# Kernel optimization log

Measured on AMD Instinct MI355X. Metric: run time of the kernel, lower is better.

Reference implementation:

```python
import jax, jax.numpy as jnp
import numpy as np

N = 20000      # nodes
E = 320000     # edges
B = 128        # graphs in batch
DIN = 64       # in_channels == out_channels (residual)
DEDGE = 64     # edge_attr_dim
DINS = 64      # ins_dim
H = 2          # heads
C = 64         # out_channels per head
L = 2          # num_ins (conv layers)
SLOPE = 0.2    # leaky relu negative slope
EPS = 1e-5     # batchnorm eps


def setup_inputs() -> dict:
    key = jax.random.key(0)
    ks = jax.random.split(key, 12)
    s = 0.05  # small glorot-ish init scale
    return {
        "x": jax.random.normal(ks[0], (N, DIN), jnp.float32),
        "edge_index": jax.random.randint(ks[1], (2, E), 0, N),
        "edge_attr": jax.random.normal(ks[2], (E, DEDGE), jnp.float32),
        "instr_vectors": jax.random.normal(ks[3], (L, B, DINS), jnp.float32),
        "batch": jnp.sort(jax.random.randint(ks[4], (N,), 0, B)),
        "W_l": jax.random.normal(ks[5], (L, DIN + DINS, H * C), jnp.float32) * s,
        "W_e": jax.random.normal(ks[6], (L, DEDGE + DINS, H * C), jnp.float32) * s,
        "att_l": jax.random.normal(ks[7], (L, H, C), jnp.float32) * s,
        "att_r": jax.random.normal(ks[8], (L, H, C), jnp.float32) * s,
        "att_e": jax.random.normal(ks[9], (L, H, C), jnp.float32) * s,
        "bias": jnp.zeros((L, C), jnp.float32),
        "bn_gamma": jnp.ones((L - 1, C), jnp.float32),
        "bn_beta": jnp.zeros((L - 1, C), jnp.float32),
    }


def reference(x, edge_index, edge_attr, instr_vectors, batch,
              W_l, W_e, att_l, att_r, att_e, bias, bn_gamma, bn_beta):
    src, dst = edge_index[0], edge_index[1]  # j -> i (source_to_target)
    h = x
    for i in range(L):
        ins = instr_vectors[i]                                   # [B, DINS]
        x_cat = jnp.concatenate([h, ins[batch]], axis=-1)        # [N, DIN+DINS]
        e_cat = jnp.concatenate([edge_attr, ins[batch[src]]], axis=-1)  # [E, ...]
        xl = (x_cat @ W_l[i]).reshape(-1, H, C)                  # [N,H,C] (lin_l == lin_r)
        al = (xl * att_l[i]).sum(-1)                             # [N,H]
        ar = (xl * att_r[i]).sum(-1)                             # [N,H]
        eh = (e_cat @ W_e[i]).reshape(-1, H, C)                  # [E,H,C]
        ae = (eh * att_e[i]).sum(-1)                             # [E,H]
        a = al[src] + ar[dst] + ae                               # [E,H]
        a = jnp.where(a > 0, a, SLOPE * a)                       # leaky relu
        # segment softmax over incoming edges of each target node
        m = jax.ops.segment_max(a, dst, num_segments=N)          # [N,H]
        ex = jnp.exp(a - m[dst])
        ssum = jax.ops.segment_sum(ex, dst, num_segments=N)
        alpha = ex / (ssum[dst] + 1e-16)                         # [E,H]
        out = jax.ops.segment_sum(xl[src] * alpha[:, :, None], dst, num_segments=N)
        out = out.mean(axis=1) + bias[i]                         # concat=False -> head mean
        h = out + h                                              # residual
        if i != L - 1:
            mu = h.mean(axis=0)
            var = ((h - mu) ** 2).mean(axis=0)                   # biased var (BN training)
            h = (h - mu) / jnp.sqrt(var + EPS) * bn_gamma[i] + bn_beta[i]
            h = jax.nn.relu(h)
    return h
```

## Files before the change

kernel.cpp:

```cpp
#include <hip/hip_runtime.h>
#include <math.h>

#define NN 20000
#define NE 320000
#define NB 128
#define SLOPE 0.2f
#define BN_EPS 1e-5f
#define NBLK 79

__device__ __forceinline__ unsigned short f2bf(float f) {
    unsigned int u = __float_as_uint(f);
    unsigned int r = (u + 0x7FFFu + ((u >> 16) & 1u)) >> 16;
    return (unsigned short)r;
}
__device__ __forceinline__ float bf2f(unsigned short h) {
    return __uint_as_float(((unsigned int)h) << 16);
}

__global__ __launch_bounds__(256) void k_hist(const int* __restrict__ dst, int* __restrict__ deg) {
    int e = blockIdx.x * 256 + threadIdx.x;
    if (e < NE) atomicAdd(&deg[dst[e]], 1);
}

__global__ __launch_bounds__(256) void k_scanA(const int* __restrict__ deg, int* __restrict__ bsum) {
    __shared__ int wsum[4];
    int t = threadIdx.x;
    int idx = blockIdx.x * 256 + t;
    int v = (idx < NN) ? deg[idx] : 0;
    for (int off = 32; off > 0; off >>= 1) v += __shfl_xor(v, off);
    if ((t & 63) == 0) wsum[t >> 6] = v;
    __syncthreads();
    if (t == 0) bsum[blockIdx.x] = wsum[0] + wsum[1] + wsum[2] + wsum[3];
}

__global__ __launch_bounds__(64) void k_scanB(const int* __restrict__ bsum, int* __restrict__ boff,
                                              int* __restrict__ rowptr) {
    int l = threadIdx.x;
    int v0 = (l < NBLK) ? bsum[l] : 0;
    int v1 = (64 + l < NBLK) ? bsum[64 + l] : 0;
    int o0 = v0, o1 = v1;
    for (int off = 1; off < 64; off <<= 1) { int u = __shfl_up(v0, off); if (l >= off) v0 += u; }
    int tot0 = __shfl(v0, 63);
    for (int off = 1; off < 64; off <<= 1) { int u = __shfl_up(v1, off); if (l >= off) v1 += u; }
    int tot1 = __shfl(v1, 63);
    if (l < NBLK) boff[l] = v0 - o0;
    if (64 + l < NBLK) boff[64 + l] = tot0 + v1 - o1;
    if (l == 0) rowptr[NN] = tot0 + tot1;
}

__global__ __launch_bounds__(256) void k_scanC(const int* __restrict__ deg, const int* __restrict__ boff,
                                               int* __restrict__ rowptr, int* __restrict__ cursor) {
    __shared__ int wsum[4];
    int t = threadIdx.x, lane = t & 63, w = t >> 6;
    int idx = blockIdx.x * 256 + t;
    int v = (idx < NN) ? deg[idx] : 0;
    int incl = v;
    for (int off = 1; off < 64; off <<= 1) { int u = __shfl_up(incl, off); if (lane >= off) incl += u; }
    if (lane == 63) wsum[w] = incl;
    __syncthreads();
    int pre = 0;
    for (int i = 0; i < w; ++i) pre += wsum[i];
    int excl = incl - v + pre + boff[blockIdx.x];
    if (idx < NN) { rowptr[idx] = excl; cursor[idx] = excl; }
}

__global__ __launch_bounds__(256) void k_p1(const float* __restrict__ We, const float* __restrict__ atte,
                                            float* __restrict__ ve01, float* __restrict__ w2e01) {
    int L = blockIdx.x;
    const float* WeL = We + (size_t)L * 128 * 128;
    const float* aeL = atte + L * 128;
    int t = threadIdx.x;
    int h = (t >> 6) & 1;
    int k = t & 63;
    int row = (t < 128) ? k : (64 + k);
    float acc = 0.f;
    for (int c = 0; c < 64; ++c) acc += WeL[row * 128 + h * 64 + c] * aeL[h * 64 + c];
    if (t < 128) ve01[L * 128 + t] = acc;
    else        w2e01[L * 128 + (t - 128)] = acc;
}

__global__ __launch_bounds__(256) void k_p2both(const float* __restrict__ instr, const float* __restrict__ Wl,
                                                const float* __restrict__ w2e01,
                                                float* __restrict__ insl01, float* __restrict__ ce01) {
    int blk = blockIdx.x, t = threadIdx.x;
    if (blk < 128) {
        int L = blk >> 6;
        int idx = (blk & 63) * 256 + t;
        int b = idx >> 7, j = idx & 127;
        const float* ins = instr + (size_t)L * NB * 64;
        const float* WlL = Wl + (size_t)L * 128 * 128;
        float acc = 0.f;
        for (int k = 0; k < 64; ++k) acc += ins[b * 64 + k] * WlL[(64 + k) * 128 + j];
        insl01[(size_t)L * 16384 + idx] = acc;
    } else {
        int L = blk - 128;
        int b = t >> 1, h = t & 1;
        const float* ins = instr + (size_t)L * NB * 64;
        const float* w2 = w2e01 + L * 128 + h * 64;
        float acc = 0.f;
        for (int k = 0; k < 64; ++k) acc += ins[b * 64 + k] * w2[k];
        ce01[L * 256 + b * 2 + h] = acc;
    }
}

__global__ __launch_bounds__(256) void k_sced(const int* __restrict__ src, const int* __restrict__ dst,
                                              const float* __restrict__ eattr, const float* __restrict__ ve01,
                                              int* __restrict__ cursor,
                                              int* __restrict__ csr_s, int* __restrict__ csr_d,
                                              float4* __restrict__ ae4) {
    __shared__ float sv[256];
    int t = threadIdx.x;
    sv[t] = ve01[t];
    __syncthreads();
    int e = blockIdx.x * 256 + t;
    if (e >= NE) return;
    int s = src[e], d = dst[e];
    const float4* row = (const float4*)(eattr + (size_t)e * 64);
    float a00 = 0.f, a01 = 0.f, a10 = 0.f, a11 = 0.f;
#pragma unroll
    for (int q = 0; q < 16; ++q) {
        float4 f = row[q];
        int k = q * 4;
        a00 += f.x * sv[k] + f.y * sv[k + 1] + f.z * sv[k + 2] + f.w * sv[k + 3];
        a01 += f.x * sv[64 + k] + f.y * sv[64 + k + 1] + f.z * sv[64 + k + 2] + f.w * sv[64 + k + 3];
        a10 += f.x * sv[128 + k] + f.y * sv[128 + k + 1] + f.z * sv[128 + k + 2] + f.w * sv[128 + k + 3];
        a11 += f.x * sv[192 + k] + f.y * sv[192 + k + 1] + f.z * sv[192 + k + 2] + f.w * sv[192 + k + 3];
    }
    int pos = atomicAdd(&cursor[d], 1);
    csr_s[pos] = s;
    csr_d[pos] = d;
    ae4[pos] = make_float4(a00, a01, a10, a11);
}

__global__ __launch_bounds__(256) void k_node(const float* __restrict__ hcur, const float* __restrict__ Wl,
                                              const float* __restrict__ insl, const int* __restrict__ batch,
                                              const float* __restrict__ attl, const float* __restrict__ attr_,
                                              const float2* __restrict__ ce2,
                                              const float* __restrict__ scsh, int use_bn,
                                              unsigned short* __restrict__ xlh,
                                              float* __restrict__ alc, float* __restrict__ ar) {
    __shared__ float sh[8 * 64];
    int t = threadIdx.x;
    int row0 = blockIdx.x * 8;
    for (int idx = t; idx < 512; idx += 256) {
        int r = idx >> 6, k = idx & 63;
        int n = row0 + r;
        float hv = (n < NN) ? hcur[n * 64 + k] : 0.f;
        if (use_bn) hv = fmaxf(hv * scsh[k] + scsh[64 + k], 0.f);
        sh[idx] = hv;
    }
    __syncthreads();
    int w = t >> 6, lane = t & 63;
    int h = w & 1;
    int rbase = (w >> 1) * 4;
    int j = h * 64 + lane;
    float attlv = attl[j];
    float attrv = attr_[j];
    float acc0 = 0.f, acc1 = 0.f, acc2 = 0.f, acc3 = 0.f;
    for (int k = 0; k < 64; ++k) {
        float wv = Wl[k * 128 + j];
        acc0 += sh[(rbase + 0) * 64 + k] * wv;
        acc1 += sh[(rbase + 1) * 64 + k] * wv;
        acc2 += sh[(rbase + 2) * 64 + k] * wv;
        acc3 += sh[(rbase + 3) * 64 + k] * wv;
    }
    float accs[4] = {acc0, acc1, acc2, acc3};
    for (int rr = 0; rr < 4; ++rr) {
        int n = row0 + rbase + rr;
        if (n >= NN) break;
        int b = batch[n];
        float v = accs[rr] + insl[b * 128 + j];
        xlh[(size_t)n * 128 + j] = f2bf(v);
        float pl = v * attlv, pr = v * attrv;
        for (int off = 32; off > 0; off >>= 1) {
            pl += __shfl_xor(pl, off);
            pr += __shfl_xor(pr, off);
        }
        if (lane == 0) {
            float2 cb = ce2[b];
            alc[n * 2 + h] = pl + (h ? cb.y : cb.x);
            ar[n * 2 + h] = pr;
        }
    }
}

__global__ __launch_bounds__(256) void k_attnexp(const int* __restrict__ csr_s, const int* __restrict__ csr_d,
                                                 const float4* __restrict__ ae4, int layer,
                                                 const float2* __restrict__ alc2, const float2* __restrict__ ar2,
                                                 int4* __restrict__ rec) {
    int p = blockIdx.x * 256 + threadIdx.x;
    if (p >= NE) return;
    int s = csr_s[p], d = csr_d[p];
    float4 ae = ae4[p];
    float2 a_l = alc2[s];
    float2 a_r = ar2[d];
    float a0 = a_l.x + a_r.x + (layer ? ae.z : ae.x);
    float a1 = a_l.y + a_r.y + (layer ? ae.w : ae.y);
    a0 = (a0 > 0.f) ? a0 : SLOPE * a0;
    a1 = (a1 > 0.f) ? a1 : SLOPE * a1;
    rec[p] = make_int4(s, __float_as_int(__expf(a0)), __float_as_int(__expf(a1)), 0);
}

__global__ __launch_bounds__(256) void k_gather(const int* __restrict__ rowptr, const int4* __restrict__ rec,
                                                const unsigned int* __restrict__ xl32,
                                                const float* __restrict__ bias, const float* __restrict__ hprev,
                                                const float* __restrict__ scsh, int use_bn,
                                                float* __restrict__ hnew) {
    int t = threadIdx.x;
    int w = t >> 6, lane = t & 63;
    int n = blockIdx.x * 4 + w;
    if (n >= NN) return;
    int r0 = rowptr[n], r1 = rowptr[n + 1];
    float acc0 = 0.f, acc1 = 0.f, ss = 0.f;
    const unsigned int* xlp = xl32 + lane;
#pragma unroll 4
    for (int p = r0; p < r1; ++p) {
        int4 r = rec[p];
        float ex = (lane < 32) ? __int_as_float(r.y) : __int_as_float(r.z);
        unsigned int pr = xlp[(size_t)r.x * 64];
        ss += ex;
        acc0 += ex * bf2f((unsigned short)(pr & 0xFFFFu));
        acc1 += ex * bf2f((unsigned short)(pr >> 16));
    }
    float inv = 1.f / (ss + 1e-16f);
    acc0 *= inv; acc1 *= inv;
    float o0 = 0.5f * (acc0 + __shfl_xor(acc0, 32));
    float o1 = 0.5f * (acc1 + __shfl_xor(acc1, 32));
    if (lane < 32) {
        float2 hv = ((const float2*)(hprev + (size_t)n * 64))[lane];
        if (use_bn) {
            float2 sc = ((const float2*)scsh)[lane];
            float2 sf = ((const float2*)(scsh + 64))[lane];
            hv.x = fmaxf(hv.x * sc.x + sf.x, 0.f);
            hv.y = fmaxf(hv.y * sc.y + sf.y, 0.f);
        }
        float2 bv = ((const float2*)bias)[lane];
        float2 o;
        o.x = o0 + bv.x + hv.x;
        o.y = o1 + bv.y + hv.y;
        ((float2*)(hnew + (size_t)n * 64))[lane] = o;
    }
}

__global__ __launch_bounds__(256) void k_bnstat(const float* __restrict__ hbuf,
                                                float* __restrict__ part, float* __restrict__ partsq) {
    __shared__ float sA[256], sB[256];
    int t = threadIdx.x;
    int c = t & 63, r = t >> 6;
    int n0 = blockIdx.x * 80;
    float s = 0.f, s2 = 0.f;
    for (int i = 0; i < 20; ++i) {
        float v = hbuf[(size_t)(n0 + i * 4 + r) * 64 + c];
        s += v; s2 += v * v;
    }
    sA[t] = s; sB[t] = s2;
    __syncthreads();
    if (t < 64) {
        part[blockIdx.x * 64 + t]   = sA[t] + sA[t + 64] + sA[t + 128] + sA[t + 192];
        partsq[blockIdx.x * 64 + t] = sB[t] + sB[t + 64] + sB[t + 128] + sB[t + 192];
    }
}

__global__ __launch_bounds__(256) void k_bnred(const float* __restrict__ part, const float* __restrict__ partsq,
                                               const float* __restrict__ gamma, const float* __restrict__ beta,
                                               float* __restrict__ scsh) {
    __shared__ float sA[256], sB[256];
    int t = threadIdx.x;
    int c = t & 63, q = t >> 6;
    float s = 0.f, s2 = 0.f;
    for (int j = q; j < 250; j += 4) { s += part[j * 64 + c]; s2 += partsq[j * 64 + c]; }
    sA[t] = s; sB[t] = s2;
    __syncthreads();
    if (t < 64) {
        float su = sA[t] + sA[t + 64] + sA[t + 128] + sA[t + 192];
        float sq = sB[t] + sB[t + 64] + sB[t + 128] + sB[t + 192];
        float mu = su * (1.f / NN);
        float var = sq * (1.f / NN) - mu * mu;
        float sc = gamma[t] * rsqrtf(var + BN_EPS);
        scsh[t] = sc;
        scsh[64 + t] = beta[t] - mu * sc;
    }
}

extern "C" void kernel_launch(void* const* d_in, const int* in_sizes, int n_in,
                              void* d_out, int out_size, void* d_ws, size_t ws_size,
                              hipStream_t stream) {
    (void)in_sizes; (void)n_in; (void)out_size; (void)ws_size;
    const float* x     = (const float*)d_in[0];
    const int*   eidx  = (const int*)d_in[1];
    const float* eattr = (const float*)d_in[2];
    const float* instr = (const float*)d_in[3];
    const int*   batch = (const int*)d_in[4];
    const float* W_l   = (const float*)d_in[5];
    const float* W_e   = (const float*)d_in[6];
    const float* att_l = (const float*)d_in[7];
    const float* att_r = (const float*)d_in[8];
    const float* att_e = (const float*)d_in[9];
    const float* bias  = (const float*)d_in[10];
    const float* bn_g  = (const float*)d_in[11];
    const float* bn_b  = (const float*)d_in[12];
    float* out = (float*)d_out;

    const int* src = eidx;
    const int* dst = eidx + NE;

    char* ws = (char*)d_ws;
    float4* ae4     = (float4*)ws;     ws += (size_t)NE * 16;
    int4*   rec     = (int4*)ws;       ws += (size_t)NE * 16;
    unsigned short* xlh = (unsigned short*)ws; ws += (size_t)NN * 128 * 2;
    int*    csr_s   = (int*)ws;        ws += (size_t)NE * 4;
    int*    csr_d   = (int*)ws;        ws += (size_t)NE * 4;
    int*    deg     = (int*)ws;        ws += NN * 4;
    int*    rowptr  = (int*)ws;        ws += (NN + 1) * 4 + 4;
    int*    cursor  = (int*)ws;        ws += NN * 4;
    int*    bsum    = (int*)ws;        ws += 80 * 4;
    int*    boff    = (int*)ws;        ws += 80 * 4;
    float*  alc     = (float*)ws;      ws += NN * 2 * 4;
    float*  ar      = (float*)ws;      ws += NN * 2 * 4;
    float*  insl01  = (float*)ws;      ws += 2 * 128 * 128 * 4;
    float*  ve01    = (float*)ws;      ws += 256 * 4;
    float*  w2e01   = (float*)ws;      ws += 256 * 4;
    float*  ce01    = (float*)ws;      ws += 2 * 256 * 4;
    float*  hbuf    = (float*)ws;      ws += (size_t)NN * 64 * 4;
    float*  part    = (float*)ws;      ws += 250 * 64 * 4;
    float*  partsq  = (float*)ws;      ws += 250 * 64 * 4;
    float*  scsh    = (float*)ws;      ws += 128 * 4;

    hipMemsetAsync(deg, 0, NN * 4, stream);
    k_hist<<<(NE + 255) / 256, 256, 0, stream>>>(dst, deg);
    k_scanA<<<NBLK, 256, 0, stream>>>(deg, bsum);
    k_scanB<<<1, 64, 0, stream>>>(bsum, boff, rowptr);
    k_scanC<<<NBLK, 256, 0, stream>>>(deg, boff, rowptr, cursor);

    k_p1<<<2, 256, 0, stream>>>(W_e, att_e, ve01, w2e01);
    k_sced<<<(NE + 255) / 256, 256, 0, stream>>>(src, dst, eattr, ve01, cursor, csr_s, csr_d, ae4);
    k_p2both<<<130, 256, 0, stream>>>(instr, W_l, w2e01, insl01, ce01);

    for (int i = 0; i < 2; ++i) {
        const float* hcur = (i == 0) ? x : hbuf;
        float* hnew = (i == 0) ? hbuf : out;
        const float* Wl_i = W_l + (size_t)i * 128 * 128;

        k_node<<<(NN + 7) / 8, 256, 0, stream>>>(hcur, Wl_i, insl01 + (size_t)i * 16384, batch,
                                                 att_l + i * 128, att_r + i * 128,
                                                 (const float2*)(ce01 + i * 256),
                                                 scsh, i, xlh, alc, ar);
        k_attnexp<<<(NE + 255) / 256, 256, 0, stream>>>(csr_s, csr_d, ae4, i,
                                                        (const float2*)alc, (const float2*)ar, rec);
        k_gather<<<NN / 4, 256, 0, stream>>>(rowptr, rec, (const unsigned int*)xlh,
                                             bias + i * 64, hcur, scsh, i, hnew);
        if (i == 0) {
            k_bnstat<<<250, 256, 0, stream>>>(hbuf, part, partsq);
            k_bnred<<<1, 256, 0, stream>>>(part, partsq, bn_g, bn_b, scsh);
        }
    }
}
```

Before: 306.5 us.

## Fuse layer-0 attention exp into CSR scatter; compact edge records to half precision

Moves the edge-scatter kernel after the layer-0 node kernel so it can compute the layer-0 attention logits and exponentials directly, removing the first attnexp pass. The edge-attribute dot products are now done cooperatively by 16 lanes per edge with coalesced float4 loads and shuffle reductions. Per-edge records shrink from 16-byte float4/int4 to 8-byte int2/float2, with exp weights stored as half2, which cuts gather and attnexp memory traffic. The trade-off is fp16 precision and possible overflow on the exp values, and a different scheduling dependency where scatter must now wait for the node kernel.

```diff
diff --git a/kernel.cpp b/kernel.cpp
--- a/kernel.cpp
+++ b/kernel.cpp
@@ -1,4 +1,5 @@
 #include <hip/hip_runtime.h>
+#include <hip/hip_fp16.h>
 #include <math.h>
 
 #define NN 20000
@@ -103,35 +104,6 @@
     }
 }
 
-__global__ __launch_bounds__(256) void k_sced(const int* __restrict__ src, const int* __restrict__ dst,
-                                              const float* __restrict__ eattr, const float* __restrict__ ve01,
-                                              int* __restrict__ cursor,
-                                              int* __restrict__ csr_s, int* __restrict__ csr_d,
-                                              float4* __restrict__ ae4) {
-    __shared__ float sv[256];
-    int t = threadIdx.x;
-    sv[t] = ve01[t];
-    __syncthreads();
-    int e = blockIdx.x * 256 + t;
-    if (e >= NE) return;
-    int s = src[e], d = dst[e];
-    const float4* row = (const float4*)(eattr + (size_t)e * 64);
-    float a00 = 0.f, a01 = 0.f, a10 = 0.f, a11 = 0.f;
-#pragma unroll
-    for (int q = 0; q < 16; ++q) {
-        float4 f = row[q];
-        int k = q * 4;
-        a00 += f.x * sv[k] + f.y * sv[k + 1] + f.z * sv[k + 2] + f.w * sv[k + 3];
-        a01 += f.x * sv[64 + k] + f.y * sv[64 + k + 1] + f.z * sv[64 + k + 2] + f.w * sv[64 + k + 3];
-        a10 += f.x * sv[128 + k] + f.y * sv[128 + k + 1] + f.z * sv[128 + k + 2] + f.w * sv[128 + k + 3];
-        a11 += f.x * sv[192 + k] + f.y * sv[192 + k + 1] + f.z * sv[192 + k + 2] + f.w * sv[192 + k + 3];
-    }
-    int pos = atomicAdd(&cursor[d], 1);
-    csr_s[pos] = s;
-    csr_d[pos] = d;
-    ae4[pos] = make_float4(a00, a01, a10, a11);
-}
-
 __global__ __launch_bounds__(256) void k_node(const float* __restrict__ hcur, const float* __restrict__ Wl,
                                               const float* __restrict__ insl, const int* __restrict__ batch,
                                               const float* __restrict__ attl, const float* __restrict__ attr_,
@@ -184,24 +156,73 @@
     }
 }
 
-__global__ __launch_bounds__(256) void k_attnexp(const int* __restrict__ csr_s, const int* __restrict__ csr_d,
-                                                 const float4* __restrict__ ae4, int layer,
+__global__ __launch_bounds__(256) void k_sced(const int* __restrict__ src, const int* __restrict__ dst,
+                                              const float* __restrict__ eattr, const float* __restrict__ ve01,
+                                              int* __restrict__ cursor,
+                                              const float2* __restrict__ alc2, const float2* __restrict__ ar2,
+                                              int2* __restrict__ csr_sd, float2* __restrict__ ae2,
+                                              int2* __restrict__ rec0) {
+    __shared__ float sv[256];
+    int t = threadIdx.x;
+    sv[t] = ve01[t];
+    __syncthreads();
+    int w = t >> 6, lane = t & 63;
+    int l16 = lane & 15, sub = lane >> 4;
+    int ebase = blockIdx.x * 256 + w * 64;
+    const float4* sv4 = (const float4*)sv;
+    float4 v0 = sv4[l16];
+    float4 v1 = sv4[16 + l16];
+    float4 v2 = sv4[32 + l16];
+    float4 v3 = sv4[48 + l16];
+    for (int it = 0; it < 16; ++it) {
+        int e = ebase + it * 4 + sub;
+        float4 f = ((const float4*)eattr)[(size_t)e * 16 + l16];
+        float d00 = f.x * v0.x + f.y * v0.y + f.z * v0.z + f.w * v0.w;
+        float d01 = f.x * v1.x + f.y * v1.y + f.z * v1.z + f.w * v1.w;
+        float d10 = f.x * v2.x + f.y * v2.y + f.z * v2.z + f.w * v2.w;
+        float d11 = f.x * v3.x + f.y * v3.y + f.z * v3.z + f.w * v3.w;
+#pragma unroll
+        for (int off = 1; off < 16; off <<= 1) {
+            d00 += __shfl_xor(d00, off);
+            d01 += __shfl_xor(d01, off);
+            d10 += __shfl_xor(d10, off);
+            d11 += __shfl_xor(d11, off);
+        }
+        if (l16 == 0) {
+            int s = src[e], dd = dst[e];
+            int pos = atomicAdd(&cursor[dd], 1);
+            csr_sd[pos] = make_int2(s, dd);
+            ae2[pos] = make_float2(d10, d11);
+            float2 a_l = alc2[s];
+            float2 a_r = ar2[dd];
+            float a0 = a_l.x + a_r.x + d00;
+            float a1 = a_l.y + a_r.y + d01;
+            a0 = (a0 > 0.f) ? a0 : SLOPE * a0;
+            a1 = (a1 > 0.f) ? a1 : SLOPE * a1;
+            __half2 hx = __floats2half2_rn(__expf(a0), __expf(a1));
+            rec0[pos] = make_int2(s, *(int*)&hx);
+        }
+    }
+}
+
+__global__ __launch_bounds__(256) void k_attnexp(const int2* __restrict__ csr_sd, const float2* __restrict__ ae2,
                                                  const float2* __restrict__ alc2, const float2* __restrict__ ar2,
-                                                 int4* __restrict__ rec) {
+                                                 int2* __restrict__ rec) {
     int p = blockIdx.x * 256 + threadIdx.x;
     if (p >= NE) return;
-    int s = csr_s[p], d = csr_d[p];
-    float4 ae = ae4[p];
-    float2 a_l = alc2[s];
-    float2 a_r = ar2[d];
-    float a0 = a_l.x + a_r.x + (layer ? ae.z : ae.x);
-    float a1 = a_l.y + a_r.y + (layer ? ae.w : ae.y);
+    int2 sd = csr_sd[p];
+    float2 ae = ae2[p];
+    float2 a_l = alc2[sd.x];
+    float2 a_r = ar2[sd.y];
+    float a0 = a_l.x + a_r.x + ae.x;
+    float a1 = a_l.y + a_r.y + ae.y;
     a0 = (a0 > 0.f) ? a0 : SLOPE * a0;
     a1 = (a1 > 0.f) ? a1 : SLOPE * a1;
-    rec[p] = make_int4(s, __float_as_int(__expf(a0)), __float_as_int(__expf(a1)), 0);
-}
-
-__global__ __launch_bounds__(256) void k_gather(const int* __restrict__ rowptr, const int4* __restrict__ rec,
+    __half2 hx = __floats2half2_rn(__expf(a0), __expf(a1));
+    rec[p] = make_int2(sd.x, *(int*)&hx);
+}
+
+__global__ __launch_bounds__(256) void k_gather(const int* __restrict__ rowptr, const int2* __restrict__ rec,
                                                 const unsigned int* __restrict__ xl32,
                                                 const float* __restrict__ bias, const float* __restrict__ hprev,
                                                 const float* __restrict__ scsh, int use_bn,
@@ -213,10 +234,12 @@
     int r0 = rowptr[n], r1 = rowptr[n + 1];
     float acc0 = 0.f, acc1 = 0.f, ss = 0.f;
     const unsigned int* xlp = xl32 + lane;
-#pragma unroll 4
+#pragma unroll 8
     for (int p = r0; p < r1; ++p) {
-        int4 r = rec[p];
-        float ex = (lane < 32) ? __int_as_float(r.y) : __int_as_float(r.z);
+        int2 r = rec[p];
+        __half2 hx = *(__half2*)&r.y;
+        float2 e2 = __half22float2(hx);
+        float ex = (lane < 32) ? e2.x : e2.y;
         unsigned int pr = xlp[(size_t)r.x * 64];
         ss += ex;
         acc0 += ex * bf2f((unsigned short)(pr & 0xFFFFu));
@@ -305,11 +328,10 @@
     const int* dst = eidx + NE;
 
     char* ws = (char*)d_ws;
-    float4* ae4     = (float4*)ws;     ws += (size_t)NE * 16;
-    int4*   rec     = (int4*)ws;       ws += (size_t)NE * 16;
+    int2*   csr_sd  = (int2*)ws;       ws += (size_t)NE * 8;
+    float2* ae2     = (float2*)ws;     ws += (size_t)NE * 8;
+    int2*   rec     = (int2*)ws;       ws += (size_t)NE * 8;
     unsigned short* xlh = (unsigned short*)ws; ws += (size_t)NN * 128 * 2;
-    int*    csr_s   = (int*)ws;        ws += (size_t)NE * 4;
-    int*    csr_d   = (int*)ws;        ws += (size_t)NE * 4;
     int*    deg     = (int*)ws;        ws += NN * 4;
     int*    rowptr  = (int*)ws;        ws += (NN + 1) * 4 + 4;
     int*    cursor  = (int*)ws;        ws += NN * 4;
@@ -333,25 +355,24 @@
     k_scanC<<<NBLK, 256, 0, stream>>>(deg, boff, rowptr, cursor);
 
     k_p1<<<2, 256, 0, stream>>>(W_e, att_e, ve01, w2e01);
-    k_sced<<<(NE + 255) / 256, 256, 0, stream>>>(src, dst, eattr, ve01, cursor, csr_s, csr_d, ae4);
     k_p2both<<<130, 256, 0, stream>>>(instr, W_l, w2e01, insl01, ce01);
 
-    for (int i = 0; i < 2; ++i) {
-        const float* hcur = (i == 0) ? x : hbuf;
-        float* hnew = (i == 0) ? hbuf : out;
-        const float* Wl_i = W_l + (size_t)i * 128 * 128;
-
-        k_node<<<(NN + 7) / 8, 256, 0, stream>>>(hcur, Wl_i, insl01 + (size_t)i * 16384, batch,
-                                                 att_l + i * 128, att_r + i * 128,
-                                                 (const float2*)(ce01 + i * 256),
-                                                 scsh, i, xlh, alc, ar);
-        k_attnexp<<<(NE + 255) / 256, 256, 0, stream>>>(csr_s, csr_d, ae4, i,
-                                                        (const float2*)alc, (const float2*)ar, rec);
-        k_gather<<<NN / 4, 256, 0, stream>>>(rowptr, rec, (const unsigned int*)xlh,
-                                             bias + i * 64, hcur, scsh, i, hnew);
-        if (i == 0) {
-            k_bnstat<<<250, 256, 0, stream>>>(hbuf, part, partsq);
-            k_bnred<<<1, 256, 0, stream>>>(part, partsq, bn_g, bn_b, scsh);
-        }
-    }
-}
+    k_node<<<(NN + 7) / 8, 256, 0, stream>>>(x, W_l, insl01, batch,
+                                             att_l, att_r, (const float2*)ce01,
+                                             scsh, 0, xlh, alc, ar);
+    k_sced<<<NE / 256, 256, 0, stream>>>(src, dst, eattr, ve01, cursor,
+                                         (const float2*)alc, (const float2*)ar,
+                                         csr_sd, ae2, rec);
+    k_gather<<<NN / 4, 256, 0, stream>>>(rowptr, rec, (const unsigned int*)xlh,
+                                         bias, x, scsh, 0, hbuf);
+    k_bnstat<<<250, 256, 0, stream>>>(hbuf, part, partsq);
+    k_bnred<<<1, 256, 0, stream>>>(part, partsq, bn_g, bn_b, scsh);
+
+    k_node<<<(NN + 7) / 8, 256, 0, stream>>>(hbuf, W_l + 128 * 128, insl01 + 16384, batch,
+                                             att_l + 128, att_r + 128, (const float2*)(ce01 + 256),
+                                             scsh, 1, xlh, alc, ar);
+    k_attnexp<<<(NE + 255) / 256, 256, 0, stream>>>(csr_sd, ae2,
+                                                    (const float2*)alc, (const float2*)ar, rec);
+    k_gather<<<NN / 4, 256, 0, stream>>>(rowptr, rec, (const unsigned int*)xlh,
+                                         bias + 64, hbuf, scsh, 1, out);
+}
```

New measurement: 308.8 us. About the same (+0.8%).

## Fuse edge attention logits into gather, pack edge records with fp16 logits

Applied to the files above, without the earlier changes.

Removes the per-layer k_attnexp pass. The edge-scatter kernel now writes a single CSR record per edge holding the source index and fp16-packed edge-attention terms for both layers. The gather kernel computes leaky-relu and exp inline, reading alc[src] and ar[dst] per edge, which drops the csr_s, csr_d and ae4 buffers and a full pass over the edges. Each sced thread now handles 4 edges. The trade-offs are fp16 precision on the edge logits and an extra random alc gather plus exp computed by every lane in the inner loop.

```diff
diff --git a/kernel.cpp b/kernel.cpp
--- a/kernel.cpp
+++ b/kernel.cpp
@@ -1,4 +1,5 @@
 #include <hip/hip_runtime.h>
+#include <hip/hip_fp16.h>
 #include <math.h>
 
 #define NN 20000
@@ -103,35 +104,6 @@
     }
 }
 
-__global__ __launch_bounds__(256) void k_sced(const int* __restrict__ src, const int* __restrict__ dst,
-                                              const float* __restrict__ eattr, const float* __restrict__ ve01,
-                                              int* __restrict__ cursor,
-                                              int* __restrict__ csr_s, int* __restrict__ csr_d,
-                                              float4* __restrict__ ae4) {
-    __shared__ float sv[256];
-    int t = threadIdx.x;
-    sv[t] = ve01[t];
-    __syncthreads();
-    int e = blockIdx.x * 256 + t;
-    if (e >= NE) return;
-    int s = src[e], d = dst[e];
-    const float4* row = (const float4*)(eattr + (size_t)e * 64);
-    float a00 = 0.f, a01 = 0.f, a10 = 0.f, a11 = 0.f;
-#pragma unroll
-    for (int q = 0; q < 16; ++q) {
-        float4 f = row[q];
-        int k = q * 4;
-        a00 += f.x * sv[k] + f.y * sv[k + 1] + f.z * sv[k + 2] + f.w * sv[k + 3];
-        a01 += f.x * sv[64 + k] + f.y * sv[64 + k + 1] + f.z * sv[64 + k + 2] + f.w * sv[64 + k + 3];
-        a10 += f.x * sv[128 + k] + f.y * sv[128 + k + 1] + f.z * sv[128 + k + 2] + f.w * sv[128 + k + 3];
-        a11 += f.x * sv[192 + k] + f.y * sv[192 + k + 1] + f.z * sv[192 + k + 2] + f.w * sv[192 + k + 3];
-    }
-    int pos = atomicAdd(&cursor[d], 1);
-    csr_s[pos] = s;
-    csr_d[pos] = d;
-    ae4[pos] = make_float4(a00, a01, a10, a11);
-}
-
 __global__ __launch_bounds__(256) void k_node(const float* __restrict__ hcur, const float* __restrict__ Wl,
                                               const float* __restrict__ insl, const int* __restrict__ batch,
                                               const float* __restrict__ attl, const float* __restrict__ attr_,
@@ -184,46 +156,71 @@
     }
 }
 
-__global__ __launch_bounds__(256) void k_attnexp(const int* __restrict__ csr_s, const int* __restrict__ csr_d,
-                                                 const float4* __restrict__ ae4, int layer,
-                                                 const float2* __restrict__ alc2, const float2* __restrict__ ar2,
-                                                 int4* __restrict__ rec) {
-    int p = blockIdx.x * 256 + threadIdx.x;
-    if (p >= NE) return;
-    int s = csr_s[p], d = csr_d[p];
-    float4 ae = ae4[p];
-    float2 a_l = alc2[s];
-    float2 a_r = ar2[d];
-    float a0 = a_l.x + a_r.x + (layer ? ae.z : ae.x);
-    float a1 = a_l.y + a_r.y + (layer ? ae.w : ae.y);
-    a0 = (a0 > 0.f) ? a0 : SLOPE * a0;
-    a1 = (a1 > 0.f) ? a1 : SLOPE * a1;
-    rec[p] = make_int4(s, __float_as_int(__expf(a0)), __float_as_int(__expf(a1)), 0);
+__global__ __launch_bounds__(256) void k_sced(const int* __restrict__ src, const int* __restrict__ dst,
+                                              const float* __restrict__ eattr, const float* __restrict__ ve01,
+                                              int* __restrict__ cursor, int4* __restrict__ rec) {
+    __shared__ float sv[256];
+    int t = threadIdx.x;
+    sv[t] = ve01[t];
+    __syncthreads();
+    const float4* sv4 = (const float4*)sv;
+#pragma unroll
+    for (int j = 0; j < 4; ++j) {
+        int e = blockIdx.x * 1024 + j * 256 + t;
+        if (e >= NE) return;
+        const float4* row = (const float4*)(eattr + (size_t)e * 64);
+        float d0 = 0.f, d1 = 0.f, d2 = 0.f, d3 = 0.f;
+#pragma unroll 4
+        for (int q = 0; q < 16; ++q) {
+            float4 f = row[q];
+            float4 u0 = sv4[q], u1 = sv4[16 + q], u2 = sv4[32 + q], u3 = sv4[48 + q];
+            d0 += f.x * u0.x + f.y * u0.y + f.z * u0.z + f.w * u0.w;
+            d1 += f.x * u1.x + f.y * u1.y + f.z * u1.z + f.w * u1.w;
+            d2 += f.x * u2.x + f.y * u2.y + f.z * u2.z + f.w * u2.w;
+            d3 += f.x * u3.x + f.y * u3.y + f.z * u3.z + f.w * u3.w;
+        }
+        int s = src[e], dd = dst[e];
+        int pos = atomicAdd(&cursor[dd], 1);
+        __half2 h01 = __floats2half2_rn(d0, d1);
+        __half2 h23 = __floats2half2_rn(d2, d3);
+        rec[pos] = make_int4(s, *(int*)&h01, *(int*)&h23, 0);
+    }
 }
 
 __global__ __launch_bounds__(256) void k_gather(const int* __restrict__ rowptr, const int4* __restrict__ rec,
                                                 const unsigned int* __restrict__ xl32,
+                                                const float2* __restrict__ alc2, const float2* __restrict__ ar2,
                                                 const float* __restrict__ bias, const float* __restrict__ hprev,
-                                                const float* __restrict__ scsh, int use_bn,
+                                                const float* __restrict__ scsh, int use_bn, int layer,
                                                 float* __restrict__ hnew) {
     int t = threadIdx.x;
     int w = t >> 6, lane = t & 63;
     int n = blockIdx.x * 4 + w;
     if (n >= NN) return;
     int r0 = rowptr[n], r1 = rowptr[n + 1];
+    float2 arn = ar2[n];
     float acc0 = 0.f, acc1 = 0.f, ss = 0.f;
     const unsigned int* xlp = xl32 + lane;
-#pragma unroll 4
+#pragma unroll 8
     for (int p = r0; p < r1; ++p) {
         int4 r = rec[p];
-        float ex = (lane < 32) ? __int_as_float(r.y) : __int_as_float(r.z);
-        unsigned int pr = xlp[(size_t)r.x * 64];
+        int s = r.x;
+        int dw = layer ? r.z : r.y;
+        __half2 hh = *(__half2*)&dw;
+        float2 d = __half22float2(hh);
+        float2 al = alc2[s];
+        float a0 = al.x + arn.x + d.x;
+        float a1 = al.y + arn.y + d.y;
+        a0 = (a0 > 0.f) ? a0 : SLOPE * a0;
+        a1 = (a1 > 0.f) ? a1 : SLOPE * a1;
+        float ex = (lane < 32) ? __expf(a0) : __expf(a1);
+        unsigned int pr = xlp[(size_t)s * 64];
         ss += ex;
         acc0 += ex * bf2f((unsigned short)(pr & 0xFFFFu));
         acc1 += ex * bf2f((unsigned short)(pr >> 16));
     }
-    float inv = 1.f / (ss + 1e-16f);
-    acc0 *= inv; acc1 *= inv;
+    float inv_s = 1.f / (ss + 1e-16f);
+    acc0 *= inv_s; acc1 *= inv_s;
     float o0 = 0.5f * (acc0 + __shfl_xor(acc0, 32));
     float o1 = 0.5f * (acc1 + __shfl_xor(acc1, 32));
     if (lane < 32) {
@@ -305,11 +302,8 @@
     const int* dst = eidx + NE;
 
     char* ws = (char*)d_ws;
-    float4* ae4     = (float4*)ws;     ws += (size_t)NE * 16;
     int4*   rec     = (int4*)ws;       ws += (size_t)NE * 16;
     unsigned short* xlh = (unsigned short*)ws; ws += (size_t)NN * 128 * 2;
-    int*    csr_s   = (int*)ws;        ws += (size_t)NE * 4;
-    int*    csr_d   = (int*)ws;        ws += (size_t)NE * 4;
     int*    deg     = (int*)ws;        ws += NN * 4;
     int*    rowptr  = (int*)ws;        ws += (NN + 1) * 4 + 4;
     int*    cursor  = (int*)ws;        ws += NN * 4;
@@ -333,25 +327,23 @@
     k_scanC<<<NBLK, 256, 0, stream>>>(deg, boff, rowptr, cursor);
 
     k_p1<<<2, 256, 0, stream>>>(W_e, att_e, ve01, w2e01);
-    k_sced<<<(NE + 255) / 256, 256, 0, stream>>>(src, dst, eattr, ve01, cursor, csr_s, csr_d, ae4);
     k_p2both<<<130, 256, 0, stream>>>(instr, W_l, w2e01, insl01, ce01);
 
-    for (int i = 0; i < 2; ++i) {
-        const float* hcur = (i == 0) ? x : hbuf;
-        float* hnew = (i == 0) ? hbuf : out;
-        const float* Wl_i = W_l + (size_t)i * 128 * 128;
-
-        k_node<<<(NN + 7) / 8, 256, 0, stream>>>(hcur, Wl_i, insl01 + (size_t)i * 16384, batch,
-                                                 att_l + i * 128, att_r + i * 128,
-                                                 (const float2*)(ce01 + i * 256),
-                                                 scsh, i, xlh, alc, ar);
-        k_attnexp<<<(NE + 255) / 256, 256, 0, stream>>>(csr_s, csr_d, ae4, i,
-                                                        (const float2*)alc, (const float2*)ar, rec);
-        k_gather<<<NN / 4, 256, 0, stream>>>(rowptr, rec, (const unsigned int*)xlh,
-                                             bias + i * 64, hcur, scsh, i, hnew);
-        if (i == 0) {
-            k_bnstat<<<250, 256, 0, stream>>>(hbuf, part, partsq);
-            k_bnred<<<1, 256, 0, stream>>>(part, partsq, bn_g, bn_b, scsh);
-        }
-    }
-}
+    k_sced<<<(NE + 1023) / 1024, 256, 0, stream>>>(src, dst, eattr, ve01, cursor, rec);
+
+    k_node<<<(NN + 7) / 8, 256, 0, stream>>>(x, W_l, insl01, batch,
+                                             att_l, att_r, (const float2*)ce01,
+                                             scsh, 0, xlh, alc, ar);
+    k_gather<<<NN / 4, 256, 0, stream>>>(rowptr, rec, (const unsigned int*)xlh,
+                                         (const float2*)alc, (const float2*)ar,
+                                         bias, x, scsh, 0, 0, hbuf);
+    k_bnstat<<<250, 256, 0, stream>>>(hbuf, part, partsq);
+    k_bnred<<<1, 256, 0, stream>>>(part, partsq, bn_g, bn_b, scsh);
+
+    k_node<<<(NN + 7) / 8, 256, 0, stream>>>(hbuf, W_l + 128 * 128, insl01 + 16384, batch,
+                                             att_l + 128, att_r + 128, (const float2*)(ce01 + 256),
+                                             scsh, 1, xlh, alc, ar);
+    k_gather<<<NN / 4, 256, 0, stream>>>(rowptr, rec, (const unsigned int*)xlh,
+                                         (const float2*)alc, (const float2*)ar,
+                                         bias + 64, hbuf, scsh, 1, 1, out);
+}
```

After: 368.2 us. +20.1%, slower.
